# Performance work log

Hardware: AMD Instinct MI355X
Metric: run time of the kernel (lower is better)

Reference implementation:

```python
import jax, jax.numpy as jnp
import numpy as np

EMBED = 512  # scale uses embed_size**-0.5 per the original forward (NOT head_size)


def setup_inputs() -> dict:
    key = jax.random.key(0)
    k1, k2, k3, k4 = jax.random.split(key, 4)
    B, T, D, H = 8, 4096, EMBED, 64
    inputs = jax.random.normal(k1, (B, T, D), dtype=jnp.float32)
    Wq = jax.random.normal(k2, (D, H), dtype=jnp.float32) * (D ** -0.5)
    Wk = jax.random.normal(k3, (D, H), dtype=jnp.float32) * (D ** -0.5)
    Wv = jax.random.normal(k4, (D, H), dtype=jnp.float32) * (D ** -0.5)
    return {"inputs": inputs, "Wq": Wq, "Wk": Wk, "Wv": Wv}


def reference(inputs, Wq, Wk, Wv):
    # inputs: [B, T, D]; Wq/Wk/Wv: [D, H]
    B, T, D = inputs.shape
    q = inputs @ Wq  # [B, T, H]
    k = inputs @ Wk  # [B, T, H]
    v = inputs @ Wv  # [B, T, H]
    scale = jnp.asarray(D, inputs.dtype) ** -0.5  # original scales by embed_size**-0.5
    scores = jnp.einsum('bth,bsh->bts', q, k) * scale  # [B, T, T]
    causal = jnp.arange(T)[:, None] >= jnp.arange(T)[None, :]  # lower-triangular
    scores = jnp.where(causal, scores, jnp.asarray(-jnp.inf, scores.dtype))
    weights = jax.nn.softmax(scores, axis=-1)
    # dropout is identity in eval mode
    return weights @ v  # [B, T, H]
```

## Files before the change

kernel.cpp:

```cpp
#include <hip/hip_runtime.h>
#include <hip/hip_bf16.h>
#include <math.h>

#define TSEQ 4096
#define NB 8
#define DEM 512
#define HD 64
#define LP 72
#define WIP 136
#define WIMG 26624
#define QSZ ((size_t)NB * TSEQ * HD)

typedef __attribute__((ext_vector_type(8))) short short8;
typedef __attribute__((ext_vector_type(4))) short short4v;
typedef __attribute__((ext_vector_type(4))) float float4v;

__device__ __forceinline__ short f2bf(float f) {
    union { float f; unsigned u; } v; v.f = f;
    unsigned r = v.u + 0x7fffu + ((v.u >> 16) & 1u);
    return (short)(r >> 16);
}

__device__ __forceinline__ short8 pack8(float4 a, float4 b) {
    union { short8 s; __hip_bfloat162 h[4]; } u;
    u.h[0] = __float22bfloat162_rn(make_float2(a.x, a.y));
    u.h[1] = __float22bfloat162_rn(make_float2(a.z, a.w));
    u.h[2] = __float22bfloat162_rn(make_float2(b.x, b.y));
    u.h[3] = __float22bfloat162_rn(make_float2(b.z, b.w));
    return u.s;
}

__device__ __forceinline__ void gload_lds16(const void* g, void* l) {
    __builtin_amdgcn_global_load_lds(
        (const __attribute__((address_space(1))) unsigned int*)g,
        (__attribute__((address_space(3))) unsigned int*)l,
        16, 0, 0);
}

__device__ __host__ __forceinline__ int slot_base(int mq) {
    int grp = mq >> 3;
    return 4 * grp * (grp + 1) + (mq & 7) * (grp + 1);
}

__global__ __launch_bounds__(256) void wtr_kernel(
    const float* __restrict__ Wq, const float* __restrict__ Wk,
    const float* __restrict__ Wv, short* __restrict__ wimg)
{
    __shared__ float t[64][65];
    const int tid = threadIdx.x;
    const int kb = blockIdx.x;
    const int k0 = kb * 64;
    const int m = blockIdx.y;
    const int c = kb >> 1, half = kb & 1;
    const float* W = (m == 0) ? Wq : ((m == 1) ? Wk : Wv);
    const float sc = (m == 0) ? 0.044194173824159216f : 1.0f;

#pragma unroll
    for (int i = 0; i < 4; ++i) {
        int f = tid + 256 * i;
        int k = f >> 4, n4 = (f & 15) * 4;
        float4 wv = *(const float4*)&W[(k0 + k) * HD + n4];
        t[k][n4 + 0] = wv.x; t[k][n4 + 1] = wv.y;
        t[k][n4 + 2] = wv.z; t[k][n4 + 3] = wv.w;
    }
    __syncthreads();
#pragma unroll
    for (int i = 0; i < 4; ++i) {
        int f = tid + 256 * i;
        int n = f >> 4, k4 = (f & 15) * 4;
        short4v o;
        o[0] = f2bf(t[k4 + 0][n] * sc);
        o[1] = f2bf(t[k4 + 1][n] * sc);
        o[2] = f2bf(t[k4 + 2][n] * sc);
        o[3] = f2bf(t[k4 + 3][n] * sc);
        *(short4v*)&wimg[c * WIMG + (64 * m + n) * WIP + half * 64 + k4] = o;
    }
}

__global__ __launch_bounds__(256, 2) void qkv_mfma(
    const float* __restrict__ x, const short* __restrict__ wimg,
    short* __restrict__ q, short* __restrict__ k, short* __restrict__ vt)
{
    __shared__ alignas(16) short wlds[WIMG];

    const int tid = threadIdx.x;
    const int w = tid >> 6;
    const int l15 = tid & 15;
    const int quad = (tid >> 4) & 3;
    const int rbase = blockIdx.x * 64 + w * 16 + l15;

    const float* xr = x + (size_t)rbase * DEM;
    float4v acc[12] = {};

    for (int c = 0; c < 4; ++c) {
        __syncthreads();
        {
            const char* gsrc = (const char*)(wimg + c * WIMG) + tid * 16;
            char* ldst = (char*)wlds + tid * 16;
#pragma unroll
            for (int i = 0; i < 13; ++i)
                gload_lds16(gsrc + i * 4096, ldst + i * 4096);
        }
        __syncthreads();

#pragma unroll
        for (int ks = 0; ks < 4; ++ks) {
            const int k0 = c * 128 + ks * 32 + quad * 8;
            float4 xa = *(const float4*)&xr[k0];
            float4 xb = *(const float4*)&xr[k0 + 4];
            short8 xv = pack8(xa, xb);
            const int lk = ks * 32 + quad * 8;
#pragma unroll
            for (int mt = 0; mt < 12; ++mt) {
                short8 wf = *(const short8*)&wlds[(mt * 16 + l15) * WIP + lk];
                acc[mt] = __builtin_amdgcn_mfma_f32_16x16x32_bf16(wf, xv, acc[mt], 0, 0, 0);
            }
        }
    }

#pragma unroll
    for (int mt = 0; mt < 8; ++mt) {
        short* dst = (mt < 4) ? q : k;
        short4v o;
        o[0] = f2bf(acc[mt][0]); o[1] = f2bf(acc[mt][1]);
        o[2] = f2bf(acc[mt][2]); o[3] = f2bf(acc[mt][3]);
        *(short4v*)&dst[(size_t)rbase * HD + (mt & 3) * 16 + quad * 4] = o;
    }
    const int b = rbase >> 12, t = rbase & (TSEQ - 1);
#pragma unroll
    for (int mt = 8; mt < 12; ++mt) {
#pragma unroll
        for (int reg = 0; reg < 4; ++reg) {
            int d = (mt - 8) * 16 + quad * 4 + reg;
            vt[((size_t)(b * HD + d)) * TSEQ + t] = f2bf(acc[mt][reg]);
        }
    }
}

__global__ __launch_bounds__(256, 4) void flash_mfma(
    const short* __restrict__ qw, const short* __restrict__ kw,
    const short* __restrict__ vtw, float* __restrict__ out,
    float* __restrict__ pO, float* __restrict__ stS)
{
    __shared__ short kt[64 * LP];
    __shared__ short vt[64 * LP];
    __shared__ short pt[4][32 * LP];

    const int tid = threadIdx.x;
    const int w = tid >> 6;
    const int l15 = tid & 15;
    const int quad = (tid >> 4) & 3;
    const int bx = blockIdx.x;
    const int b = bx & 7;
    const int idx = bx >> 3;

    int mq, j;
    if (idx < 52) {
        int t = idx;
        mq = 31; j = 0;
#pragma unroll 1
        for (int mm = 31; mm >= 7; --mm) {
            int f = (2 * mm + 2) >> 4;
            if (t < f) { mq = mm; j = t; break; }
            t -= f;
        }
    } else {
        int t = idx - 52;
        int kc = t >> 2, p = t & 3;
        mq = 30 - kc - 8 * p;
        j = (2 * mq + 2) >> 4;
    }
    const int s0 = 16 * j;
    const int send = min(16 * (j + 1), 2 * mq + 2);
    const int r0 = mq * 128;
    const int slot = b * 80 + slot_base(mq) + j;

    short8 qf[2][2];
#pragma unroll
    for (int g = 0; g < 2; ++g) {
        const short* qrow = qw + ((size_t)(b * TSEQ + r0 + 32 * w + 16 * g + l15)) * HD;
        qf[g][0] = *(const short8*)(qrow + quad * 8);
        qf[g][1] = *(const short8*)(qrow + 32 + quad * 8);
    }

    float l_lane[2] = {0.f, 0.f};
    float4v O[2][4] = {};

    const int srow = tid >> 3, sc = tid & 7;
    const short* kbase = kw + (size_t)b * TSEQ * HD;
    const short* vbase = vtw + (size_t)b * HD * TSEQ;

    short8 kr0, kr1, vr0, vr1;
    {
        const short* kg = kbase + (size_t)(s0 * 64) * HD;
        const short* vg = vbase + s0 * 64;
        kr0 = *(const short8*)(kg + srow * HD + sc * 8);
        kr1 = *(const short8*)(kg + (srow + 32) * HD + sc * 8);
        vr0 = *(const short8*)(vg + (size_t)srow * TSEQ + sc * 8);
        vr1 = *(const short8*)(vg + (size_t)(srow + 32) * TSEQ + sc * 8);
    }

    for (int st = s0; st < send; ++st) {
        __syncthreads();
        *(short8*)&kt[srow * LP + sc * 8] = kr0;
        *(short8*)&kt[(srow + 32) * LP + sc * 8] = kr1;
        *(short8*)&vt[srow * LP + sc * 8] = vr0;
        *(short8*)&vt[(srow + 32) * LP + sc * 8] = vr1;
        __syncthreads();

        if (st + 1 < send) {
            const short* kg = kbase + (size_t)((st + 1) * 64) * HD;
            const short* vg = vbase + (st + 1) * 64;
            kr0 = *(const short8*)(kg + srow * HD + sc * 8);
            kr1 = *(const short8*)(kg + (srow + 32) * HD + sc * 8);
            vr0 = *(const short8*)(vg + (size_t)srow * TSEQ + sc * 8);
            vr1 = *(const short8*)(vg + (size_t)(srow + 32) * TSEQ + sc * 8);
        }

        float4v S[2][4] = {};
#pragma unroll
        for (int mt = 0; mt < 4; ++mt) {
            short8 a0 = *(const short8*)&kt[(mt * 16 + l15) * LP + quad * 8];
            short8 a1 = *(const short8*)&kt[(mt * 16 + l15) * LP + 32 + quad * 8];
            S[0][mt] = __builtin_amdgcn_mfma_f32_16x16x32_bf16(a0, qf[0][0], S[0][mt], 0, 0, 0);
            S[0][mt] = __builtin_amdgcn_mfma_f32_16x16x32_bf16(a1, qf[0][1], S[0][mt], 0, 0, 0);
            S[1][mt] = __builtin_amdgcn_mfma_f32_16x16x32_bf16(a0, qf[1][0], S[1][mt], 0, 0, 0);
            S[1][mt] = __builtin_amdgcn_mfma_f32_16x16x32_bf16(a1, qf[1][1], S[1][mt], 0, 0, 0);
        }

        if (st >= 2 * mq) {
            const int kb2 = st * 64;
#pragma unroll
            for (int g = 0; g < 2; ++g) {
                int qg = r0 + 32 * w + 16 * g + l15;
#pragma unroll
                for (int mt = 0; mt < 4; ++mt)
#pragma unroll
                    for (int r = 0; r < 4; ++r)
                        if (kb2 + mt * 16 + quad * 4 + r > qg) S[g][mt][r] = -INFINITY;
            }
        }

#pragma unroll
        for (int g = 0; g < 2; ++g) {
#pragma unroll
            for (int mt = 0; mt < 4; ++mt) {
                float p0 = __expf(S[g][mt][0]);
                float p1 = __expf(S[g][mt][1]);
                float p2 = __expf(S[g][mt][2]);
                float p3 = __expf(S[g][mt][3]);
                l_lane[g] += (p0 + p1) + (p2 + p3);
                short4v pk;
                pk[0] = f2bf(p0); pk[1] = f2bf(p1);
                pk[2] = f2bf(p2); pk[3] = f2bf(p3);
                *(short4v*)&pt[w][(16 * g + l15) * LP + mt * 16 + quad * 4] = pk;
            }
        }

#pragma unroll
        for (int kf = 0; kf < 2; ++kf) {
            short8 pa0 = *(const short8*)&pt[w][l15 * LP + kf * 32 + quad * 8];
            short8 pa1 = *(const short8*)&pt[w][(16 + l15) * LP + kf * 32 + quad * 8];
#pragma unroll
            for (int nt = 0; nt < 4; ++nt) {
                short8 vb = *(const short8*)&vt[(nt * 16 + l15) * LP + kf * 32 + quad * 8];
                O[0][nt] = __builtin_amdgcn_mfma_f32_16x16x32_bf16(pa0, vb, O[0][nt], 0, 0, 0);
                O[1][nt] = __builtin_amdgcn_mfma_f32_16x16x32_bf16(pa1, vb, O[1][nt], 0, 0, 0);
            }
        }
    }

    float lred[2];
#pragma unroll
    for (int g = 0; g < 2; ++g) {
        float rs = l_lane[g];
        rs += __shfl_xor(rs, 16, 64);
        rs += __shfl_xor(rs, 32, 64);
        lred[g] = rs;
    }

    if (mq <= 7) {
#pragma unroll
        for (int g = 0; g < 2; ++g) {
            float iv = 1.0f / lred[g];
#pragma unroll
            for (int r = 0; r < 4; ++r) {
                float ir = __shfl(iv, quad * 4 + r, 64);
                size_t row = (size_t)(b * TSEQ + r0 + 32 * w + 16 * g + quad * 4 + r) * HD;
#pragma unroll
                for (int nt = 0; nt < 4; ++nt)
                    out[row + nt * 16 + l15] = O[g][nt][r] * ir;
            }
        }
    } else {
        float* dest = pO + (size_t)slot * 128 * HD;
#pragma unroll
        for (int g = 0; g < 2; ++g) {
#pragma unroll
            for (int r = 0; r < 4; ++r) {
                size_t row = (size_t)(32 * w + 16 * g + quad * 4 + r) * HD;
#pragma unroll
                for (int nt = 0; nt < 4; ++nt)
                    dest[row + nt * 16 + l15] = O[g][nt][r];
            }
            if (quad == 0) stS[slot * 128 + 32 * w + 16 * g + l15] = lred[g];
        }
    }
}

__global__ __launch_bounds__(256) void merge_kernel(
    float* __restrict__ out, const float* __restrict__ pO,
    const float* __restrict__ stS)
{
    const int tid = threadIdx.x;
    const int bx = blockIdx.x;
    const int b = bx / 48, loc = bx - b * 48;
    const int t = 1024 + loc * 64 + (tid >> 2);
    const int dq = (tid & 3) * 16;
    const int mq = t >> 7, rr = t & 127;
    const int nseg = (2 * mq + 2 + 15) >> 4;
    const int sb = b * 80 + slot_base(mq);

    float denom = 0.f;
    for (int s = 0; s < nseg; ++s) denom += stS[(sb + s) * 128 + rr];
    float inv = 1.0f / denom;

    float4 o[4] = {};
    for (int s = 0; s < nseg; ++s) {
        const float4* pp = (const float4*)
            &pO[((size_t)(sb + s) * 128 + rr) * HD + dq];
#pragma unroll
        for (int i = 0; i < 4; ++i) {
            float4 p = pp[i];
            o[i].x += p.x; o[i].y += p.y;
            o[i].z += p.z; o[i].w += p.w;
        }
    }
    float4* op = (float4*)&out[((size_t)b * TSEQ + t) * HD + dq];
#pragma unroll
    for (int i = 0; i < 4; ++i) {
        o[i].x *= inv; o[i].y *= inv; o[i].z *= inv; o[i].w *= inv;
        op[i] = o[i];
    }
}

extern "C" void kernel_launch(void* const* d_in, const int* in_sizes, int n_in,
                              void* d_out, int out_size, void* d_ws, size_t ws_size,
                              hipStream_t stream) {
    const float* x  = (const float*)d_in[0];
    const float* Wq = (const float*)d_in[1];
    const float* Wk = (const float*)d_in[2];
    const float* Wv = (const float*)d_in[3];
    float* out = (float*)d_out;

    short* q  = (short*)d_ws;
    short* k  = q + QSZ;
    short* vt = k + QSZ;
    short* wimg = vt + QSZ;
    float* pO = (float*)(wimg + 4 * WIMG);
    float* stS = pO + (size_t)640 * 128 * HD;

    wtr_kernel<<<dim3(8, 3), 256, 0, stream>>>(Wq, Wk, Wv, wimg);
    qkv_mfma<<<dim3(NB * TSEQ / 64), 256, 0, stream>>>(x, wimg, q, k, vt);
    flash_mfma<<<dim3(640), 256, 0, stream>>>(q, k, vt, out, pO, stS);
    merge_kernel<<<dim3(384), 256, 0, stream>>>(out, pO, stS);
}
```

Before: 160.9 us.

## Halve KV split chunk size, add MFMA priority hints, use packed bf16 convert

Key tiles per work item drop from 16 to 8, so the split-KV schedule now produces 144 slots per batch instead of 80. The work mapping, slot layout and merge range are reworked to match, giving finer load balance across the 256 CUs. The cost is more partial-output traffic and a larger merge pass. The change also raises wave priority around the MFMA blocks with s_setprio and replaces the manual bf16 rounding with packed bf16 conversion intrinsics.

```diff
diff --git a/kernel.cpp b/kernel.cpp
--- a/kernel.cpp
+++ b/kernel.cpp
@@ -10,6 +10,7 @@
 #define WIP 136
 #define WIMG 26624
 #define QSZ ((size_t)NB * TSEQ * HD)
+#define SLOTS_PER_B 144
 
 typedef __attribute__((ext_vector_type(8))) short short8;
 typedef __attribute__((ext_vector_type(4))) short short4v;
@@ -38,8 +39,8 @@
 }
 
 __device__ __host__ __forceinline__ int slot_base(int mq) {
-    int grp = mq >> 3;
-    return 4 * grp * (grp + 1) + (mq & 7) * (grp + 1);
+    int a = mq >> 2, r = mq & 3;
+    return (a + 1) * (2 * a + r);
 }
 
 __global__ __launch_bounds__(256) void wtr_kernel(
@@ -155,25 +156,25 @@
     const int idx = bx >> 3;
 
     int mq, j;
-    if (idx < 52) {
+    if (idx < 120) {
         int t = idx;
         mq = 31; j = 0;
 #pragma unroll 1
-        for (int mm = 31; mm >= 7; --mm) {
-            int f = (2 * mm + 2) >> 4;
+        for (int mm = 31; mm >= 3; --mm) {
+            int f = (mm + 1) >> 2;
             if (t < f) { mq = mm; j = t; break; }
             t -= f;
         }
     } else {
-        int t = idx - 52;
-        int kc = t >> 2, p = t & 3;
-        mq = 30 - kc - 8 * p;
-        j = (2 * mq + 2) >> 4;
-    }
-    const int s0 = 16 * j;
-    const int send = min(16 * (j + 1), 2 * mq + 2);
+        int t = idx - 120;
+        int kc = t >> 3, p = t & 7;
+        mq = (30 - kc) - 4 * p;
+        j = (mq + 1) >> 2;
+    }
+    const int s0 = 8 * j;
+    const int send = min(8 * (j + 1), 2 * mq + 2);
     const int r0 = mq * 128;
-    const int slot = b * 80 + slot_base(mq) + j;
+    const int slot = b * SLOTS_PER_B + slot_base(mq) + j;
 
     short8 qf[2][2];
 #pragma unroll
@@ -218,6 +219,7 @@
         }
 
         float4v S[2][4] = {};
+        __builtin_amdgcn_s_setprio(1);
 #pragma unroll
         for (int mt = 0; mt < 4; ++mt) {
             short8 a0 = *(const short8*)&kt[(mt * 16 + l15) * LP + quad * 8];
@@ -227,6 +229,7 @@
             S[1][mt] = __builtin_amdgcn_mfma_f32_16x16x32_bf16(a0, qf[1][0], S[1][mt], 0, 0, 0);
             S[1][mt] = __builtin_amdgcn_mfma_f32_16x16x32_bf16(a1, qf[1][1], S[1][mt], 0, 0, 0);
         }
+        __builtin_amdgcn_s_setprio(0);
 
         if (st >= 2 * mq) {
             const int kb2 = st * 64;
@@ -250,13 +253,14 @@
                 float p2 = __expf(S[g][mt][2]);
                 float p3 = __expf(S[g][mt][3]);
                 l_lane[g] += (p0 + p1) + (p2 + p3);
-                short4v pk;
-                pk[0] = f2bf(p0); pk[1] = f2bf(p1);
-                pk[2] = f2bf(p2); pk[3] = f2bf(p3);
-                *(short4v*)&pt[w][(16 * g + l15) * LP + mt * 16 + quad * 4] = pk;
-            }
-        }
-
+                union { short4v s; __hip_bfloat162 h[2]; } pk;
+                pk.h[0] = __float22bfloat162_rn(make_float2(p0, p1));
+                pk.h[1] = __float22bfloat162_rn(make_float2(p2, p3));
+                *(short4v*)&pt[w][(16 * g + l15) * LP + mt * 16 + quad * 4] = pk.s;
+            }
+        }
+
+        __builtin_amdgcn_s_setprio(1);
 #pragma unroll
         for (int kf = 0; kf < 2; ++kf) {
             short8 pa0 = *(const short8*)&pt[w][l15 * LP + kf * 32 + quad * 8];
@@ -268,6 +272,7 @@
                 O[1][nt] = __builtin_amdgcn_mfma_f32_16x16x32_bf16(pa1, vb, O[1][nt], 0, 0, 0);
             }
         }
+        __builtin_amdgcn_s_setprio(0);
     }
 
     float lred[2];
@@ -279,7 +284,7 @@
         lred[g] = rs;
     }
 
-    if (mq <= 7) {
+    if (mq <= 3) {
 #pragma unroll
         for (int g = 0; g < 2; ++g) {
             float iv = 1.0f / lred[g];
@@ -314,12 +319,12 @@
 {
     const int tid = threadIdx.x;
     const int bx = blockIdx.x;
-    const int b = bx / 48, loc = bx - b * 48;
-    const int t = 1024 + loc * 64 + (tid >> 2);
+    const int b = bx / 56, loc = bx - b * 56;
+    const int t = 512 + loc * 64 + (tid >> 2);
     const int dq = (tid & 3) * 16;
     const int mq = t >> 7, rr = t & 127;
-    const int nseg = (2 * mq + 2 + 15) >> 4;
-    const int sb = b * 80 + slot_base(mq);
+    const int nseg = (mq + 4) >> 2;
+    const int sb = b * SLOTS_PER_B + slot_base(mq);
 
     float denom = 0.f;
     for (int s = 0; s < nseg; ++s) denom += stS[(sb + s) * 128 + rr];
@@ -358,10 +363,10 @@
     short* vt = k + QSZ;
     short* wimg = vt + QSZ;
     float* pO = (float*)(wimg + 4 * WIMG);
-    float* stS = pO + (size_t)640 * 128 * HD;
+    float* stS = pO + (size_t)NB * SLOTS_PER_B * 128 * HD;
 
     wtr_kernel<<<dim3(8, 3), 256, 0, stream>>>(Wq, Wk, Wv, wimg);
     qkv_mfma<<<dim3(NB * TSEQ / 64), 256, 0, stream>>>(x, wimg, q, k, vt);
-    flash_mfma<<<dim3(640), 256, 0, stream>>>(q, k, vt, out, pO, stS);
-    merge_kernel<<<dim3(384), 256, 0, stream>>>(out, pO, stS);
-}
+    flash_mfma<<<dim3(NB * SLOTS_PER_B), 256, 0, stream>>>(q, k, vt, out, pO, stS);
+    merge_kernel<<<dim3(448), 256, 0, stream>>>(out, pO, stS);
+}
```

Measured after the change: 161.4 us. Within noise of the previous version (+0.3%).
